# Performance work log

Hardware: AMD Instinct MI355X
Metric: run time of the kernel (lower is better)

Reference implementation:

```python
import jax, jax.numpy as jnp
import numpy as np
from jax import lax

NUM_HOP = 2      # opt.num_hop
POOL_HOP = 1     # Encoder(..., num_hop=1) in gnn_pools
K_POOL = 1024    # int(pooling_ratio * num_patches) = 0.5 * 2048
TH = 0.0         # opt.nonzero_th
T = 0.07         # NCE temperature
NEG_FILL = -10.0


def l2norm(x):
    # Normalize(power=2): x / (sum(x^2, dim=1, keepdim)^(1/2))
    return x / jnp.sqrt(jnp.sum(x * x, axis=1, keepdims=True))


def tagconv(A, h, W, b, k):
    # DGL TAGConv: concat_{i=0..k} (D^-1/2 A D^-1/2)^i h, then linear
    deg = jnp.sum(A, axis=1)
    dinv = lax.rsqrt(jnp.maximum(deg, 1e-12))
    An = A * dinv[:, None] * dinv[None, :]   # [N,N] normalized adjacency
    feats = [h]
    for _ in range(k):
        h = An @ h
        feats.append(h)
    return jnp.concatenate(feats, axis=1) @ W + b


def nce_pair(f_t, f_s):
    # calc_gnn NCE: positives = diag(f_t . f_s); negatives = full gram with diag masked to -10
    n = f_t.shape[0]
    eye = jnp.eye(n, dtype=bool)
    pos = jnp.sum(f_t * f_s, axis=1, keepdims=True)          # [N,1]
    neg_s = jnp.where(eye, NEG_FILL, f_t @ f_s.T)            # [N,N]
    neg_t = jnp.where(eye, NEG_FILL, f_s @ f_t.T)
    out_s = jnp.concatenate([pos, neg_s], axis=1) / T
    out_t = jnp.concatenate([pos, neg_t], axis=1) / T
    # CrossEntropy with label 0 == -log_softmax(out)[:, 0], mean over rows
    loss_s = -jnp.mean(jax.nn.log_softmax(out_s, axis=1)[:, 0])
    loss_t = -jnp.mean(jax.nn.log_softmax(out_t, axis=1)[:, 0])
    return loss_s + loss_t


def setup_inputs() -> dict:
    key = jax.random.key(0)
    ks = jax.random.split(key, 8)
    N, C, D = 2048, 512, 128
    g = 0.02  # init_gain ('normal' init)
    return {
        "fs": jax.random.normal(ks[0], (N, C), jnp.float32),
        "ft": jax.random.normal(ks[1], (N, C), jnp.float32),
        "W_embed": g * jax.random.normal(ks[2], (C, D), jnp.float32),
        "b_embed": jnp.zeros((D,), jnp.float32),
        "W_gnn": g * jax.random.normal(ks[3], ((NUM_HOP + 1) * D, D), jnp.float32),
        "b_gnn": jnp.zeros((D,), jnp.float32),
        "W_pool": g * jax.random.normal(ks[4], (D, 1), jnp.float32),
        "b_pool": jnp.zeros((1,), jnp.float32),
        "W_gnnp": g * jax.random.normal(ks[5], ((POOL_HOP + 1) * D, D), jnp.float32),
        "b_gnnp": jnp.zeros((D,), jnp.float32),
    }


def reference(fs, ft, W_embed, b_embed, W_gnn, b_gnn, W_pool, b_pool, W_gnnp, b_gnnp):
    # Embed: linear + l2 norm
    f_es = l2norm(fs @ W_embed + b_embed)   # student [N, nc]
    f_et = l2norm(ft @ W_embed + b_embed)   # teacher [N, nc]

    # nonzero_graph on detached teacher features; same adjacency reused for student
    ft_d = lax.stop_gradient(f_et)
    n = f_et.shape[0]
    eye = jnp.eye(n, dtype=bool)
    A = (ft_d @ ft_d.T > TH).astype(f_et.dtype)
    A = jnp.where(eye, 1.0, A)  # dgl.add_self_loop

    # TAGConv encoder + l2norm; teacher branch detached
    f_gt = lax.stop_gradient(l2norm(tagconv(A, f_et, W_gnn, b_gnn, NUM_HOP)))
    f_gs = l2norm(tagconv(A, f_es, W_gnn, b_gnn, NUM_HOP))
    loss_g = nce_pair(f_gt, f_gs)

    # Pool / top_k_graph
    scores = jax.nn.sigmoid((f_gt @ W_pool + b_pool)[:, 0])   # [N]
    vals, idx = lax.top_k(scores, K_POOL)
    new_ht = f_gt[idx] * vals[:, None]
    new_hs = f_gs[idx] * vals[:, None]
    un = (A > 0).astype(A.dtype)
    un2 = ((un @ un) > 0).astype(A.dtype)        # 2-hop boolean adjacency
    sub = un2[idx][:, idx]                       # [k,k]
    deg = jnp.sum(sub, axis=1)
    g_pool = sub / deg[None, :]                  # replicates torch broadcast in norm_g(g/degrees)

    # pooled-stage Encoder (TAGConv k=1) on the pooled graph structure (with self loops)
    k = K_POOL
    eye_k = jnp.eye(k, dtype=bool)
    Ap = (g_pool > 0).astype(A.dtype)
    Ap = jnp.where(eye_k, 1.0, Ap)
    f_pt = lax.stop_gradient(l2norm(tagconv(Ap, new_ht, W_gnnp, b_gnnp, POOL_HOP)))
    f_ps = l2norm(tagconv(Ap, new_hs, W_gnnp, b_gnnp, POOL_HOP))
    loss_pool = nce_pair(f_pt, f_ps)

    return loss_g + loss_pool
```

## Files before the change

kernel.cpp:

```cpp
#include <hip/hip_runtime.h>


#define TINV (1.0f / 0.07f)

using short8 = __attribute__((ext_vector_type(8))) short;
using f32x4  = __attribute__((ext_vector_type(4))) float;

__device__ __forceinline__ unsigned short f2bf(float f) {
    unsigned u = __float_as_uint(f);
    u += 0x7fff + ((u >> 16) & 1);
    return (unsigned short)(u >> 16);
}

template<bool BT>
__device__ __forceinline__ void mm_tile(const float* __restrict__ A, int lda,
                                        const float* __restrict__ B, int ldb,
                                        int i0, int j0, int k0, int k1,
                                        float (&acc)[4][4],
                                        float (&As)[16][68], float (&Bs)[16][68])
{
    const int tid = threadIdx.x;
    const int tx = tid & 15;
    const int ty = tid >> 4;
    const int lr = tid >> 2;
    const int lc = (tid & 3) * 4;
    for (int k = k0; k < k1; k += 16) {
        float4 av = *(const float4*)(A + (size_t)(i0 + lr) * lda + (k + lc));
        As[lc + 0][lr] = av.x; As[lc + 1][lr] = av.y;
        As[lc + 2][lr] = av.z; As[lc + 3][lr] = av.w;
        if (BT) {
            float4 bv = *(const float4*)(B + (size_t)(j0 + lr) * ldb + (k + lc));
            Bs[lc + 0][lr] = bv.x; Bs[lc + 1][lr] = bv.y;
            Bs[lc + 2][lr] = bv.z; Bs[lc + 3][lr] = bv.w;
        } else {
            const int n = tid & 63;
            const int kb = tid >> 6;
#pragma unroll
            for (int it = 0; it < 4; ++it)
                Bs[kb * 4 + it][n] = B[(size_t)(k + kb * 4 + it) * ldb + (j0 + n)];
        }
        __syncthreads();
#pragma unroll
        for (int kk = 0; kk < 16; ++kk) {
            float a[4], b[4];
#pragma unroll
            for (int u = 0; u < 4; ++u) a[u] = As[kk][ty * 4 + u];
#pragma unroll
            for (int v = 0; v < 4; ++v) b[v] = Bs[kk][tx * 4 + v];
#pragma unroll
            for (int u = 0; u < 4; ++u)
#pragma unroll
                for (int v = 0; v < 4; ++v)
                    acc[u][v] = fmaf(a[u], b[v], acc[u][v]);
// ... 70 lines not shown
    const int i0 = by * 64, j0 = bx * 64;
    float acc[4][4] = {};
    mm_tile<true>(f_e, 128, f_e, 128, i0, j0, 0, 128, acc, As, Bs);
    const int tid = threadIdx.x;
    const int tx = tid & 15, ty = tid >> 4;
    unsigned pb = 0;
#pragma unroll
    for (int u = 0; u < 4; ++u)
#pragma unroll
        for (int v = 0; v < 4; ++v) {
            bool pred = (acc[u][v] > 0.0f) || (i0 + ty * 4 + u == j0 + tx * 4 + v);
            pb |= (unsigned)pred << (u * 4 + v);
        }
#pragma unroll
    for (int u = 0; u < 4; ++u) nib[ty * 4 + u][tx] = (pb >> (4 * u)) & 15;
#pragma unroll
    for (int v = 0; v < 4; ++v) {
        unsigned nt = 0;
#pragma unroll
        for (int u = 0; u < 4; ++u) nt |= ((pb >> (u * 4 + v)) & 1u) << u;
        nibT[tx * 4 + v][ty] = nt;
    }
    __syncthreads();
    if (tid < 64) {
        unsigned long long c = 0;
#pragma unroll
        for (int t = 0; t < 16; ++t) c |= (unsigned long long)nib[tid][t] << (4 * t);
        chk[tid] = c;
        bits[(size_t)(i0 + tid) * 32 + (j0 >> 6)] = c;
        atomicAdd(&deg[i0 + tid], __popcll(c));
    } else if (tid < 128 && bx != by) {
        const int r = tid - 64;
        unsigned long long c = 0;
#pragma unroll
        for (int t = 0; t < 16; ++t) c |= (unsigned long long)nibT[r][t] << (4 * t);
        chkT[r] = c;
        bits[(size_t)(j0 + r) * 32 + (i0 >> 6)] = c;
        atomicAdd(&deg[j0 + r], __popcll(c));
    }
    __syncthreads();
#pragma unroll
    for (int it = 0; it < 16; ++it) {
        const int row = it * 4 + (tid >> 6);
        const int col = tid & 63;
        A01[(size_t)(i0 + row) * 2048 + j0 + col] =
            ((chk[row] >> col) & 1) ? (unsigned short)0x3F80 : (unsigned short)0;
        if (bx != by)
            A01[(size_t)(j0 + row) * 2048 + i0 + col] =
                ((chkT[row] >> col) & 1) ? (unsigned short)0x3F80 : (unsigned short)0;
    }
}

__launch_bounds__(256)
__global__ void mm_bf16(const unsigned short* __restrict__ A, int lda, size_t aZ,
                        const unsigned short* __restrict__ B, int ldb, size_t bZ,
                        float* __restrict__ C, int ldc, size_t cZ,
                        int Kc, int kZ)
{
    __shared__ unsigned short As[64][40];
    __shared__ unsigned short Bs[128][40];
    const int tid = threadIdx.x;
    const int bz = blockIdx.z;
    const int i0 = blockIdx.y * 64;
    const int j0 = blockIdx.x * 128;
    const int k0 = bz * kZ;
    const unsigned short* Ab = A + (size_t)bz * aZ;
    const unsigned short* Bb = B + (size_t)bz * bZ;
    float* Cb = C + (size_t)bz * cZ;
    const int w = tid >> 6;
    const int lane = tid & 63;
    const int m = lane & 15;
    const int q = lane >> 4;
    f32x4 acc[8];
#pragma unroll
    for (int t = 0; t < 8; ++t)
#pragma unroll
        for (int r = 0; r < 4; ++r) acc[t][r] = 0.0f;

    const int ar = tid >> 2;
    const int ac = (tid & 3) * 8;
    for (int ks = 0; ks < Kc; ks += 32) {
        const int k = k0 + ks;
        *(ulonglong2*)&As[ar][ac] =
            *(const ulonglong2*)(Ab + (size_t)(i0 + ar) * lda + k + ac);
        *(ulonglong2*)&Bs[ar][ac] =
            *(const ulonglong2*)(Bb + (size_t)(j0 + ar) * ldb + k + ac);
        *(ulonglong2*)&Bs[ar + 64][ac] =
            *(const ulonglong2*)(Bb + (size_t)(j0 + ar + 64) * ldb + k + ac);
        __syncthreads();
        short8 a = *(const short8*)&As[w * 16 + m][q * 8];
#pragma unroll
        for (int nt = 0; nt < 8; ++nt) {
            short8 b = *(const short8*)&Bs[nt * 16 + m][q * 8];
            acc[nt] = __builtin_amdgcn_mfma_f32_16x16x32_bf16(a, b, acc[nt], 0, 0, 0);
        }
        __syncthreads();
    }
#pragma unroll
    for (int nt = 0; nt < 8; ++nt) {
        const int col = j0 + nt * 16 + m;
#pragma unroll
        for (int r = 0; r < 4; ++r) {
            const int row = i0 + w * 16 + q * 4 + r;
            Cb[(size_t)row * ldc + col] = acc[nt][r];
        }
    }
}

__global__ void reduce_hop(const float* __restrict__ part, int nz, size_t zstr,
                           int M, const float* __restrict__ dinv,
                           unsigned short* __restrict__ hb,
                           unsigned short* __restrict__ xt)
{
    __shared__ float T[32][33];
    const int tid = threadIdx.x;
    const int iloc = tid >> 3, nq = (tid & 7) * 4;
    const int n = blockIdx.x * 32 + nq;
    const int i = blockIdx.y * 32 + iloc;
    float4 s = *(const float4*)(part + (size_t)i * 256 + n);
    for (int z = 1; z < nz; ++z) {
        float4 t = *(const float4*)(part + (size_t)z * zstr + (size_t)i * 256 + n);
        s.x += t.x; s.y += t.y; s.z += t.z; s.w += t.w;
    }
    const float d = dinv[i];
    unsigned short o[4] = { f2bf(s.x * d), f2bf(s.y * d), f2bf(s.z * d), f2bf(s.w * d) };
    const int hrow = (n >= 128 ? M : 0) + i;
    *(ulonglong1*)(hb + (size_t)hrow * 128 + (n & 127)) = *(ulonglong1*)o;
    if (xt) {
        const float d2 = d * d;
        T[nq + 0][iloc] = s.x * d2; T[nq + 1][iloc] = s.y * d2;
        T[nq + 2][iloc] = s.z * d2; T[nq + 3][iloc] = s.w * d2;
        __syncthreads();
        const int nloc = tid >> 3, ic = (tid & 7) * 4;
        unsigned short o2[4];
#pragma unroll
        for (int c = 0; c < 4; ++c) o2[c] = f2bf(T[nloc][ic + c]);
        *(ulonglong1*)(xt + (size_t)(blockIdx.x * 32 + nloc) * M + blockIdx.y * 32 + ic) =
            *(ulonglong1*)o2;
    }
}

__global__ void combine_norm(const float* __restrict__ part, int nz, size_t zstr,
                             const float* __restrict__ bias,
                             float* __restrict__ f32out,
                             unsigned short* __restrict__ bf16out,
                             const float* __restrict__ Wp, const float* __restrict__ bp,
                             float* __restrict__ scores)
{
    const int row = blockIdx.x;
    const int tid = threadIdx.x;
    float v = bias[tid];
    for (int z = 0; z < nz; ++z) v += part[(size_t)z * zstr + (size_t)row * 128 + tid];
    __shared__ float red[128];
    red[tid] = v * v;
    __syncthreads();
    for (int s = 64; s > 0; s >>= 1) {
        if (tid < s) red[tid] += red[tid + s];
        __syncthreads();
    }
    const float o = v * (1.0f / sqrtf(red[0]));
    if (f32out)  f32out[(size_t)row * 128 + tid] = o;
    if (bf16out) bf16out[(size_t)row * 128 + tid] = f2bf(o);
    if (scores && row < 2048) {
        __syncthreads();
        red[tid] = o * Wp[tid];
        __syncthreads();
        for (int s = 64; s > 0; s >>= 1) {
            if (tid < s) red[tid] += red[tid + s];
            __syncthreads();
        }
        if (tid == 0) scores[row] = 1.0f / (1.0f + expf(-(red[0] + bp[0])));
    }
}

__global__ void make_xt(const float* __restrict__ f_e, const int* __restrict__ deg,
                        unsigned short* __restrict__ xt, float* __restrict__ dinv)
{
    __shared__ float T[32][33];
    const int b = blockIdx.x;
    const int bx = b & 7, by = b >> 3;
    const int tid = threadIdx.x;
    const int iloc = tid >> 3, nq = (tid & 7) * 4;
    const int n0 = bx * 32;
    const int i = by * 32 + iloc;
    const int srow = (n0 >= 128 ? 2048 : 0) + i;
    float4 f = *(const float4*)(f_e + (size_t)srow * 128 + ((n0 + nq) & 127));
    const float d = 1.0f / sqrtf((float)deg[i]);
    if (bx == 0 && (tid & 7) == 0) dinv[i] = d;
    T[nq + 0][iloc] = f.x * d; T[nq + 1][iloc] = f.y * d;
    T[nq + 2][iloc] = f.z * d; T[nq + 3][iloc] = f.w * d;
    __syncthreads();
    const int nloc = tid >> 3, ic = (tid & 7) * 4;
    unsigned short o[4];
#pragma unroll
    for (int c = 0; c < 4; ++c) o[c] = f2bf(T[nloc][ic + c]);
    *(ulonglong1*)(xt + (size_t)(n0 + nloc) * 2048 + by * 32 + ic) = *(ulonglong1*)o;
}

__launch_bounds__(256)
__global__ void k_nce_topk(const unsigned short* __restrict__ A,
                           const unsigned short* __restrict__ B,
                           float* __restrict__ rowsum, float* __restrict__ colsum,
                           float* __restrict__ pos, int gramBlocks, int bw,
                           const float* __restrict__ scores,
                           float* __restrict__ vals, int* __restrict__ idx)
{
    __shared__ unsigned short As[64][40];
    __shared__ unsigned short Bs[128][40];
    __shared__ float colbuf[4][128];
    __shared__ unsigned sv[2048];
    __shared__ int hist[256];
    __shared__ int shp, shr, sh_base, sh_out, wsum[5];
    const int tid = threadIdx.x;
    const int b = blockIdx.x;
    if (b < gramBlocks) {
        const int bx = b % bw, by = b / bw;
        const int i0 = by * 64;
        const int j0 = bx * 128;
        const int w = tid >> 6;
        const int lane = tid & 63;
        const int m = lane & 15;
        const int q = lane >> 4;
        f32x4 acc[8];
#pragma unroll
        for (int t = 0; t < 8; ++t)
#pragma unroll
            for (int r = 0; r < 4; ++r) acc[t][r] = 0.0f;
        const int ar = tid >> 2;
        const int ac = (tid & 3) * 8;
        for (int k = 0; k < 128; k += 32) {
            *(ulonglong2*)&As[ar][ac] =
                *(const ulonglong2*)(A + (size_t)(i0 + ar) * 128 + k + ac);
            *(ulonglong2*)&Bs[ar][ac] =
                *(const ulonglong2*)(B + (size_t)(j0 + ar) * 128 + k + ac);
            *(ulonglong2*)&Bs[ar + 64][ac] =
                *(const ulonglong2*)(B + (size_t)(j0 + ar + 64) * 128 + k + ac);
            __syncthreads();
            short8 a = *(const short8*)&As[w * 16 + m][q * 8];
#pragma unroll
            for (int nt = 0; nt < 8; ++nt) {
                short8 bb = *(const short8*)&Bs[nt * 16 + m][q * 8];
                acc[nt] = __builtin_amdgcn_mfma_f32_16x16x32_bf16(a, bb, acc[nt], 0, 0, 0);
            }
            __syncthreads();
        }
        float rpart[4] = {0.0f, 0.0f, 0.0f, 0.0f};
        float cpart[8];
#pragma unroll
        for (int nt = 0; nt < 8; ++nt) {
            const int col = j0 + nt * 16 + m;
            float cs = 0.0f;
#pragma unroll
            for (int r = 0; r < 4; ++r) {
                const int row = i0 + w * 16 + q * 4 + r;
                float g = acc[nt][r];
                float e = __expf(g * TINV);
                if (row == col) { pos[row] = g; e = 0.0f; }
                rpart[r] += e;
                cs += e;
            }
            cpart[nt] = cs;
        }
#pragma unroll
        for (int r = 0; r < 4; ++r) {
            float v = rpart[r];
            v += __shfl_xor(v, 1); v += __shfl_xor(v, 2);
            v += __shfl_xor(v, 4); v += __shfl_xor(v, 8);
            if (m == 0) atomicAdd(&rowsum[i0 + w * 16 + q * 4 + r], v);
        }
#pragma unroll
        for (int nt = 0; nt < 8; ++nt) {
            float v = cpart[nt];
            v += __shfl_xor(v, 16); v += __shfl_xor(v, 32);
            if (q == 0) colbuf[w][nt * 16 + m] = v;
        }
        __syncthreads();
        if (tid < 128) {
            float v = colbuf[0][tid] + colbuf[1][tid] + colbuf[2][tid] + colbuf[3][tid];
            atomicAdd(&colsum[j0 + tid], v);
        }
    } else {
        for (int e = tid; e < 2048; e += 256) sv[e] = __float_as_uint(scores[e]);
        if (tid == 0) { shp = 0; shr = 1024; sh_base = 0; sh_out = 0; }
        __syncthreads();
        for (int byte = 3; byte >= 0; --byte) {
            hist[tid] = 0;
            __syncthreads();
            const unsigned pref = (unsigned)shp;
            const unsigned pmask = (byte == 3) ? 0u : (0xFFFFFFFFu << ((byte + 1) * 8));
            for (int e = tid; e < 2048; e += 256) {
                unsigned u = sv[e];
                if ((u & pmask) == (pref & pmask))
                    atomicAdd(&hist[(u >> (byte * 8)) & 255], 1);
            }
            __syncthreads();
            if (tid == 0) {
                int rem = shr, bs = 255;
                for (; bs > 0; --bs) {
                    if (hist[bs] >= rem) break;
                    rem -= hist[bs];
                }
                shp = (int)(pref | ((unsigned)bs << (byte * 8)));
                shr = rem;
            }
            __syncthreads();
        }
        const unsigned t = (unsigned)shp;
        const int remain = shr;
        const int lane = tid & 63, wave = tid >> 6;
        for (int pass = 0; pass < 8; ++pass) {
            const int e = pass * 256 + tid;
            const unsigned u = sv[e];
            const bool eq = (u == t);
            unsigned long long mk = __ballot(eq);
            int wpre = __popcll(mk & ((1ull << lane) - 1ull));
            if (lane == 0) wsum[wave] = __popcll(mk);
            __syncthreads();
            if (tid == 0) {
                int a = sh_base;
                for (int ww = 0; ww < 4; ++ww) { int c = wsum[ww]; wsum[ww] = a; a += c; }
                sh_base = a;
            }
            __syncthreads();
            const int rank = eq ? (wsum[wave] + wpre) : 0x7fffffff;
            if ((u > t) || (eq && rank < remain)) {
                int slot = atomicAdd(&sh_out, 1);
                idx[slot] = e;
                vals[slot] = __uint_as_float(u);
            }
            __syncthreads();
        }
    }
}

__global__ void k_final_ap(const float* __restrict__ rs, const float* __restrict__ cs,
                           const float* __restrict__ pos, float* __restrict__ out,
                           const unsigned long long* __restrict__ bits,
                           const int* __restrict__ idx,
                           unsigned short* __restrict__ Ap, int* __restrict__ degp)
{
    __shared__ unsigned long long pb[16][33];
    __shared__ unsigned long long qb[16][33];
    __shared__ float red[256];
    const int b = blockIdx.x;
    const int tid = threadIdx.x;
    if (b < 4096) {
        const int tp = (b >> 6) * 16;
        const int tq = (b & 63) * 16;
        for (int t = tid; t < 512; t += 256) {
            int r = t >> 5, w = t & 31;
            pb[r][w] = bits[(size_t)idx[tp + r] * 32 + w];
            qb[r][w] = bits[(size_t)idx[tq + r] * 32 + w];
        }
        __syncthreads();
        const int pi = tid >> 4, qi = tid & 15;
        unsigned long long acc = 0;
#pragma unroll
        for (int w = 0; w < 32; ++w) acc |= (pb[pi][w] & qb[qi][w]);
        Ap[(size_t)(tp + pi) * 1024 + tq + qi] =
            acc ? (unsigned short)0x3F80 : (unsigned short)0;
        int v = acc ? 1 : 0;
        v += __shfl_xor(v, 1); v += __shfl_xor(v, 2);
        v += __shfl_xor(v, 4); v += __shfl_xor(v, 8);
        if (qi == 0) atomicAdd(&degp[tp + pi], v);
    } else {
        const int i = (b - 4096) * 256 + tid;
        float p = pos[i] * TINV;
        float ep = __expf(p);
        float t = (logf(rs[i] + ep) - p) + (logf(cs[i] + ep) - p);
        red[tid] = t;
        __syncthreads();
        for (int s = 128; s > 0; s >>= 1) {
            if (tid < s) red[tid] += red[tid + s];
            __syncthreads();
        }
        if (tid == 0) atomicAdd(out, red[0] * (1.0f / 2048.0f));
    }
}

__global__ void nce_final(const float* __restrict__ rs, const float* __restrict__ cs,
                          const float* __restrict__ pos, float invN,
                          float* __restrict__ out)
{
    const int i = blockIdx.x * 256 + threadIdx.x;
    float p = pos[i] * TINV;
    float ep = __expf(p);
    float t = (logf(rs[i] + ep) - p) + (logf(cs[i] + ep) - p);
    __shared__ float red[256];
    red[threadIdx.x] = t;
    __syncthreads();
    for (int s = 128; s > 0; s >>= 1) {
        if (threadIdx.x < s) red[threadIdx.x] += red[threadIdx.x + s];
        __syncthreads();
    }
    if (threadIdx.x == 0) atomicAdd(out, red[0] * invN);
}

__global__ void gather_xt(const float* __restrict__ f_g, const int* __restrict__ idx,
                          const float* __restrict__ vals, const int* __restrict__ degp,
                          unsigned short* __restrict__ new_hb,
                          unsigned short* __restrict__ xtp, float* __restrict__ dinvp)
{
    __shared__ float T[32][33];
    const int b = blockIdx.x;
    const int bx = b & 7, by = b >> 3;
    const int tid = threadIdx.x;
    const int ploc = tid >> 3, nq = (tid & 7) * 4;
    const int n0 = bx * 32;
    const int p = by * 32 + ploc;
    const int s = idx[p];
    const float v = vals[p];
    const float dp = 1.0f / sqrtf((float)degp[p]);
    if (bx == 0 && (tid & 7) == 0) dinvp[p] = dp;
    const int srow = (n0 >= 128 ? 2048 : 0) + s;
    float4 f = *(const float4*)(f_g + (size_t)srow * 128 + ((n0 + nq) & 127));
    f.x *= v; f.y *= v; f.z *= v; f.w *= v;
    unsigned short o[4] = { f2bf(f.x), f2bf(f.y), f2bf(f.z), f2bf(f.w) };
    const int hrow = (n0 >= 128 ? 1024 : 0) + p;
    *(ulonglong1*)(new_hb + (size_t)hrow * 128 + ((n0 + nq) & 127)) = *(ulonglong1*)o;
    T[nq + 0][ploc] = f.x * dp; T[nq + 1][ploc] = f.y * dp;
    T[nq + 2][ploc] = f.z * dp; T[nq + 3][ploc] = f.w * dp;
    __syncthreads();
    const int nloc = tid >> 3, pc = (tid & 7) * 4;
    unsigned short o2[4];
#pragma unroll
    for (int c = 0; c < 4; ++c) o2[c] = f2bf(T[nloc][pc + c]);
    *(ulonglong1*)(xtp + (size_t)(n0 + nloc) * 1024 + by * 32 + pc) = *(ulonglong1*)o2;
}

extern "C" void kernel_launch(void* const* d_in, const int* in_sizes, int n_in,
                              void* d_out, int out_size, void* d_ws, size_t ws_size,
                              hipStream_t stream)
{
    (void)in_sizes; (void)n_in; (void)out_size; (void)ws_size;
    const float* fs      = (const float*)d_in[0];
    const float* ft      = (const float*)d_in[1];
    const float* W_embed = (const float*)d_in[2];
    const float* b_embed = (const float*)d_in[3];
    const float* W_gnn   = (const float*)d_in[4];
    const float* b_gnn   = (const float*)d_in[5];
    const float* W_pool  = (const float*)d_in[6];
    const float* b_pool  = (const float*)d_in[7];
    const float* W_gnnp  = (const float*)d_in[8];
    const float* b_gnnp  = (const float*)d_in[9];
    float* out = (float*)d_out;

    float* ws = (float*)d_ws;
    size_t o = 0;
    auto alloc = [&](size_t n) { float* p = ws + o; o += (n + 3) & ~3ull; return p; };
    float* bigB   = alloc(2048ull * 2048);
    float* f_e    = alloc(4096 * 128);
    float* f_g    = alloc(4096 * 128);
    unsigned short* A01  = (unsigned short*)alloc(2048ull * 2048 / 2);
    unsigned short* febT = (unsigned short*)alloc(3ull * 4096 * 128 / 2);
    unsigned short* Xt1  = (unsigned short*)alloc(256ull * 2048 / 2);
    unsigned short* Xt2  = (unsigned short*)alloc(256ull * 2048 / 2);
    unsigned short* f_gb = (unsigned short*)alloc(4096ull * 128 / 2);
    unsigned short* Wtall= (unsigned short*)alloc(5ull * 16384 / 2);
    unsigned short* Ap01 = (unsigned short*)alloc(1024ull * 1024 / 2);
    unsigned short* nhb  = (unsigned short*)alloc(2ull * 2048 * 128 / 2);
    unsigned short* Xtp  = (unsigned short*)alloc(256ull * 1024 / 2);
    unsigned short* f_pb = (unsigned short*)alloc(2048ull * 128 / 2);
    float* dinv   = alloc(2048);
    float* scores = alloc(2048);
    float* vals   = alloc(1024);
    int*   idxb   = (int*)alloc(1024);
    float* dinvp  = alloc(1024);
    unsigned long long* bits = (unsigned long long*)alloc(2048 * 32 * 2);
    float* nceb = alloc(9216);
    int*   deg  = (int*)alloc(2048);
    int*   degp = (int*)alloc(1024);
    const int kZeroCount = 9216 + 2048 + 1024;

    const size_t FSTR = 4096ull * 128;
    const size_t PSTR = 1024ull * 256;
    unsigned short* feb = febT;
    unsigned short* h1b = febT + FSTR;
    unsigned short* h2b = febT + 2 * FSTR;
    unsigned short* tmpb = nhb + 2048ull * 128;
    unsigned short* Wt  = Wtall;
    unsigned short* WtP = Wtall + 3ull * 16384;
    float* rs  = nceb;
    float* csu = nceb + 2048;
    float* pos = nceb + 4096;
    float* rsp  = nceb + 6144;
    float* csp  = nceb + 7168;
    float* posp = nceb + 8192;

    k_setup_embed<<<601, 256, 0, stream>>>(fs, ft, W_embed, bigB, FSTR,
                                           (int*)nceb, kZeroCount, out, W_gnn, W_gnnp, Wtall);
    combine_norm<<<4096, 128, 0, stream>>>(bigB, 4, FSTR, b_embed, f_e, feb,
                                           nullptr, nullptr, nullptr);
    k_gram_fused<<<528, 256, 0, stream>>>(f_e, A01, bits, deg);
    make_xt<<<512, 256, 0, stream>>>(f_e, deg, Xt1, dinv);
    mm_bf16<<<dim3(2, 32, 8), 256, 0, stream>>>(A01, 2048, 0, Xt1, 2048, 0,
                                                bigB, 256, FSTR, 256, 256);
    reduce_hop<<<dim3(8, 64), 256, 0, stream>>>(bigB, 8, FSTR, 2048, dinv, h1b, Xt2);
    mm_bf16<<<dim3(2, 32, 8), 256, 0, stream>>>(A01, 2048, 0, Xt2, 2048, 0,
                                                bigB, 256, FSTR, 256, 256);
    reduce_hop<<<dim3(8, 64), 256, 0, stream>>>(bigB, 8, FSTR, 2048, dinv, h2b, nullptr);
    mm_bf16<<<dim3(1, 64, 3), 256, 0, stream>>>(feb, 128, FSTR, Wt, 128, 16384,
                                                bigB, 128, FSTR, 128, 0);
    combine_norm<<<4096, 128, 0, stream>>>(bigB, 3, FSTR, b_gnn, f_g, f_gb,
                                           W_pool, b_pool, scores);
    k_nce_topk<<<513, 256, 0, stream>>>(f_gb, f_gb + 2048 * 128, rs, csu, pos,
                                        512, 16, scores, vals, idxb);
    k_final_ap<<<4104, 256, 0, stream>>>(rs, csu, pos, out, bits, idxb, Ap01, degp);
    gather_xt<<<256, 256, 0, stream>>>(f_g, idxb, vals, degp, nhb, Xtp, dinvp);
    mm_bf16<<<dim3(2, 16, 8), 256, 0, stream>>>(Ap01, 1024, 0, Xtp, 1024, 0,
                                                bigB, 256, PSTR, 128, 128);
    reduce_hop<<<dim3(8, 32), 256, 0, stream>>>(bigB, 8, PSTR, 1024, dinvp, tmpb, nullptr);
    mm_bf16<<<dim3(1, 32, 2), 256, 0, stream>>>(nhb, 128, 2048ull * 128, WtP, 128, 16384,
                                                bigB, 128, PSTR, 128, 0);
    combine_norm<<<2048, 128, 0, stream>>>(bigB, 2, PSTR, b_gnnp, nullptr, f_pb,
                                           nullptr, nullptr, nullptr);
    k_nce_topk<<<128, 256, 0, stream>>>(f_pb, f_pb + 1024 * 128, rsp, csp, posp,
                                        128, 8, nullptr, nullptr, nullptr);
    nce_final<<<4, 256, 0, stream>>>(rsp, csp, posp, 1.0f / 1024.0f, out);
}
```

Baseline: 227.3 us.

## Fuse pooled-stage kernels into one cooperative persistent kernel with grid syncs

Replaces the seven small kernels of the pooled stage (gather, adjacency matmul, hop reduction, weight matmul, normalize, NCE gram, final reduction) with one cooperative kernel of 256 blocks that separates the phases with grid.sync(). The aim is to remove per-kernel launch gaps and tail latency on stages that are each tiny. In exchange the phases run on a fixed 256-block grid with some blocks idle, grid-wide barriers add their own cost, and the launch requires cooperative co-residency. The NCE gram tile code is also moved into a shared device function.

```diff
diff --git a/kernel.cpp b/kernel.cpp
--- a/kernel.cpp
+++ b/kernel.cpp
@@ -1,4 +1,7 @@
 #include <hip/hip_runtime.h>
+#include <hip/hip_cooperative_groups.h>
+
+namespace cg = cooperative_groups;
 
 
 #define TINV (1.0f / 0.07f)
@@ -320,11 +323,86 @@
     *(ulonglong1*)(xt + (size_t)(n0 + nloc) * 2048 + by * 32 + ic) = *(ulonglong1*)o;
 }
 
+__device__ __forceinline__ void nce_gram_tile(const unsigned short* __restrict__ A,
+                                              const unsigned short* __restrict__ B,
+                                              int i0, int j0,
+                                              float* __restrict__ rowsum,
+                                              float* __restrict__ colsum,
+                                              float* __restrict__ pos,
+                                              unsigned short (&As)[64][40],
+                                              unsigned short (&Bs)[128][40],
+                                              float (&colbuf)[4][128])
+{
+    const int tid = threadIdx.x;
+    const int w = tid >> 6;
+    const int lane = tid & 63;
+    const int m = lane & 15;
+    const int q = lane >> 4;
+    f32x4 acc[8];
+#pragma unroll
+    for (int t = 0; t < 8; ++t)
+#pragma unroll
+        for (int r = 0; r < 4; ++r) acc[t][r] = 0.0f;
+    const int ar = tid >> 2;
+    const int ac = (tid & 3) * 8;
+    for (int k = 0; k < 128; k += 32) {
+        *(ulonglong2*)&As[ar][ac] =
+            *(const ulonglong2*)(A + (size_t)(i0 + ar) * 128 + k + ac);
+        *(ulonglong2*)&Bs[ar][ac] =
+            *(const ulonglong2*)(B + (size_t)(j0 + ar) * 128 + k + ac);
+        *(ulonglong2*)&Bs[ar + 64][ac] =
+            *(const ulonglong2*)(B + (size_t)(j0 + ar + 64) * 128 + k + ac);
+        __syncthreads();
+        short8 a = *(const short8*)&As[w * 16 + m][q * 8];
+#pragma unroll
+        for (int nt = 0; nt < 8; ++nt) {
+            short8 bb = *(const short8*)&Bs[nt * 16 + m][q * 8];
+            acc[nt] = __builtin_amdgcn_mfma_f32_16x16x32_bf16(a, bb, acc[nt], 0, 0, 0);
+        }
+        __syncthreads();
+    }
+    float rpart[4] = {0.0f, 0.0f, 0.0f, 0.0f};
+    float cpart[8];
+#pragma unroll
+    for (int nt = 0; nt < 8; ++nt) {
+        const int col = j0 + nt * 16 + m;
+        float cs = 0.0f;
+#pragma unroll
+        for (int r = 0; r < 4; ++r) {
+            const int row = i0 + w * 16 + q * 4 + r;
+            float g = acc[nt][r];
+            float e = __expf(g * TINV);
+            if (row == col) { pos[row] = g; e = 0.0f; }
+            rpart[r] += e;
+            cs += e;
+        }
+        cpart[nt] = cs;
+    }
+#pragma unroll
+    for (int r = 0; r < 4; ++r) {
+        float v = rpart[r];
+        v += __shfl_xor(v, 1); v += __shfl_xor(v, 2);
+        v += __shfl_xor(v, 4); v += __shfl_xor(v, 8);
+        if (m == 0) atomicAdd(&rowsum[i0 + w * 16 + q * 4 + r], v);
+    }
+#pragma unroll
+    for (int nt = 0; nt < 8; ++nt) {
+        float v = cpart[nt];
+        v += __shfl_xor(v, 16); v += __shfl_xor(v, 32);
+        if (q == 0) colbuf[w][nt * 16 + m] = v;
+    }
+    __syncthreads();
+    if (tid < 128) {
+        float v = colbuf[0][tid] + colbuf[1][tid] + colbuf[2][tid] + colbuf[3][tid];
+        atomicAdd(&colsum[j0 + tid], v);
+    }
+}
+
 __launch_bounds__(256)
 __global__ void k_nce_topk(const unsigned short* __restrict__ A,
                            const unsigned short* __restrict__ B,
                            float* __restrict__ rowsum, float* __restrict__ colsum,
-                           float* __restrict__ pos, int gramBlocks, int bw,
+                           float* __restrict__ pos,
                            const float* __restrict__ scores,
                            float* __restrict__ vals, int* __restrict__ idx)
 {
@@ -336,72 +414,9 @@
     __shared__ int shp, shr, sh_base, sh_out, wsum[5];
     const int tid = threadIdx.x;
     const int b = blockIdx.x;
-    if (b < gramBlocks) {
-        const int bx = b % bw, by = b / bw;
-        const int i0 = by * 64;
-        const int j0 = bx * 128;
-        const int w = tid >> 6;
-        const int lane = tid & 63;
-        const int m = lane & 15;
-        const int q = lane >> 4;
-        f32x4 acc[8];
-#pragma unroll
-        for (int t = 0; t < 8; ++t)
-#pragma unroll
-            for (int r = 0; r < 4; ++r) acc[t][r] = 0.0f;
-        const int ar = tid >> 2;
-        const int ac = (tid & 3) * 8;
-        for (int k = 0; k < 128; k += 32) {
-            *(ulonglong2*)&As[ar][ac] =
-                *(const ulonglong2*)(A + (size_t)(i0 + ar) * 128 + k + ac);
-            *(ulonglong2*)&Bs[ar][ac] =
-                *(const ulonglong2*)(B + (size_t)(j0 + ar) * 128 + k + ac);
-            *(ulonglong2*)&Bs[ar + 64][ac] =
-                *(const ulonglong2*)(B + (size_t)(j0 + ar + 64) * 128 + k + ac);
-            __syncthreads();
-            short8 a = *(const short8*)&As[w * 16 + m][q * 8];
-#pragma unroll
-            for (int nt = 0; nt < 8; ++nt) {
-                short8 bb = *(const short8*)&Bs[nt * 16 + m][q * 8];
-                acc[nt] = __builtin_amdgcn_mfma_f32_16x16x32_bf16(a, bb, acc[nt], 0, 0, 0);
-            }
-            __syncthreads();
-        }
-        float rpart[4] = {0.0f, 0.0f, 0.0f, 0.0f};
-        float cpart[8];
-#pragma unroll
-        for (int nt = 0; nt < 8; ++nt) {
-            const int col = j0 + nt * 16 + m;
-            float cs = 0.0f;
-#pragma unroll
-            for (int r = 0; r < 4; ++r) {
-                const int row = i0 + w * 16 + q * 4 + r;
-                float g = acc[nt][r];
-                float e = __expf(g * TINV);
-                if (row == col) { pos[row] = g; e = 0.0f; }
-                rpart[r] += e;
-                cs += e;
-            }
-            cpart[nt] = cs;
-        }
-#pragma unroll
-        for (int r = 0; r < 4; ++r) {
-            float v = rpart[r];
-            v += __shfl_xor(v, 1); v += __shfl_xor(v, 2);
-            v += __shfl_xor(v, 4); v += __shfl_xor(v, 8);
-            if (m == 0) atomicAdd(&rowsum[i0 + w * 16 + q * 4 + r], v);
-        }
-#pragma unroll
-        for (int nt = 0; nt < 8; ++nt) {
-            float v = cpart[nt];
-            v += __shfl_xor(v, 16); v += __shfl_xor(v, 32);
-            if (q == 0) colbuf[w][nt * 16 + m] = v;
-        }
-        __syncthreads();
-        if (tid < 128) {
-            float v = colbuf[0][tid] + colbuf[1][tid] + colbuf[2][tid] + colbuf[3][tid];
-            atomicAdd(&colsum[j0 + tid], v);
-        }
+    if (b < 512) {
+        nce_gram_tile(A, B, (b / 16) * 64, (b % 16) * 128, rowsum, colsum, pos,
+                      As, Bs, colbuf);
     } else {
         for (int e = tid; e < 2048; e += 256) sv[e] = __float_as_uint(scores[e]);
         if (tid == 0) { shp = 0; shr = 1024; sh_base = 0; sh_out = 0; }
@@ -501,54 +516,188 @@
     }
 }
 
-__global__ void nce_final(const float* __restrict__ rs, const float* __restrict__ cs,
-                          const float* __restrict__ pos, float invN,
-                          float* __restrict__ out)
-{
-    const int i = blockIdx.x * 256 + threadIdx.x;
-    float p = pos[i] * TINV;
-    float ep = __expf(p);
-    float t = (logf(rs[i] + ep) - p) + (logf(cs[i] + ep) - p);
+__launch_bounds__(256)
+__global__ void k_pooled(const float* __restrict__ f_g, const int* __restrict__ idx,
+                         const float* __restrict__ vals, const int* __restrict__ degp,
+                         unsigned short* __restrict__ new_hb,
+                         unsigned short* __restrict__ xtp,
+                         float* __restrict__ dinvp,
+                         const unsigned short* __restrict__ Ap,
+                         float* __restrict__ partb,
+                         unsigned short* __restrict__ tmpb,
+                         const unsigned short* __restrict__ WtP,
+                         const float* __restrict__ bgp,
+                         unsigned short* __restrict__ f_pb,
+                         float* __restrict__ rsp, float* __restrict__ csp,
+                         float* __restrict__ posp, float* __restrict__ out)
+{
+    cg::grid_group grid = cg::this_grid();
+    __shared__ unsigned short As[64][40];
+    __shared__ unsigned short Bs[128][40];
+    __shared__ float colbuf[4][128];
+    __shared__ float T[32][33];
     __shared__ float red[256];
-    red[threadIdx.x] = t;
-    __syncthreads();
-    for (int s = 128; s > 0; s >>= 1) {
-        if (threadIdx.x < s) red[threadIdx.x] += red[threadIdx.x + s];
-        __syncthreads();
-    }
-    if (threadIdx.x == 0) atomicAdd(out, red[0] * invN);
-}
-
-__global__ void gather_xt(const float* __restrict__ f_g, const int* __restrict__ idx,
-                          const float* __restrict__ vals, const int* __restrict__ degp,
-                          unsigned short* __restrict__ new_hb,
-                          unsigned short* __restrict__ xtp, float* __restrict__ dinvp)
-{
-    __shared__ float T[32][33];
     const int b = blockIdx.x;
-    const int bx = b & 7, by = b >> 3;
-    const int tid = threadIdx.x;
-    const int ploc = tid >> 3, nq = (tid & 7) * 4;
-    const int n0 = bx * 32;
-    const int p = by * 32 + ploc;
-    const int s = idx[p];
-    const float v = vals[p];
-    const float dp = 1.0f / sqrtf((float)degp[p]);
-    if (bx == 0 && (tid & 7) == 0) dinvp[p] = dp;
-    const int srow = (n0 >= 128 ? 2048 : 0) + s;
-    float4 f = *(const float4*)(f_g + (size_t)srow * 128 + ((n0 + nq) & 127));
-    f.x *= v; f.y *= v; f.z *= v; f.w *= v;
-    unsigned short o[4] = { f2bf(f.x), f2bf(f.y), f2bf(f.z), f2bf(f.w) };
-    const int hrow = (n0 >= 128 ? 1024 : 0) + p;
-    *(ulonglong1*)(new_hb + (size_t)hrow * 128 + ((n0 + nq) & 127)) = *(ulonglong1*)o;
-    T[nq + 0][ploc] = f.x * dp; T[nq + 1][ploc] = f.y * dp;
-    T[nq + 2][ploc] = f.z * dp; T[nq + 3][ploc] = f.w * dp;
-    __syncthreads();
-    const int nloc = tid >> 3, pc = (tid & 7) * 4;
-    unsigned short o2[4];
-#pragma unroll
-    for (int c = 0; c < 4; ++c) o2[c] = f2bf(T[nloc][pc + c]);
-    *(ulonglong1*)(xtp + (size_t)(n0 + nloc) * 1024 + by * 32 + pc) = *(ulonglong1*)o2;
+    const int tid = threadIdx.x;
+    const size_t PSTR = 1024ull * 256;
+
+    {
+        const int bx = b & 7, by = b >> 3;
+        const int ploc = tid >> 3, nq = (tid & 7) * 4;
+        const int n0 = bx * 32;
+        const int p = by * 32 + ploc;
+        const int s = idx[p];
+        const float v = vals[p];
+        const float dp = 1.0f / sqrtf((float)degp[p]);
+        if (bx == 0 && (tid & 7) == 0) dinvp[p] = dp;
+        const int srow = (n0 >= 128 ? 2048 : 0) + s;
+        float4 f = *(const float4*)(f_g + (size_t)srow * 128 + ((n0 + nq) & 127));
+        f.x *= v; f.y *= v; f.z *= v; f.w *= v;
+        unsigned short o[4] = { f2bf(f.x), f2bf(f.y), f2bf(f.z), f2bf(f.w) };
+        const int hrow = (n0 >= 128 ? 1024 : 0) + p;
+        *(ulonglong1*)(new_hb + (size_t)hrow * 128 + ((n0 + nq) & 127)) = *(ulonglong1*)o;
+        T[nq + 0][ploc] = f.x * dp; T[nq + 1][ploc] = f.y * dp;
+        T[nq + 2][ploc] = f.z * dp; T[nq + 3][ploc] = f.w * dp;
+        __syncthreads();
+        const int nloc = tid >> 3, pc = (tid & 7) * 4;
+        unsigned short o2[4];
+#pragma unroll
+        for (int c = 0; c < 4; ++c) o2[c] = f2bf(T[nloc][pc + c]);
+        *(ulonglong1*)(xtp + (size_t)(n0 + nloc) * 1024 + by * 32 + pc) = *(ulonglong1*)o2;
+    }
+    grid.sync();
+
+    {
+        const int bx = b & 1, by = (b >> 1) & 15, bz = b >> 5;
+        const int i0 = by * 64, j0 = bx * 128, k0 = bz * 128;
+        float* Cb = partb + (size_t)bz * PSTR;
+        const int w = tid >> 6, lane = tid & 63, m = lane & 15, q = lane >> 4;
+        f32x4 acc[8];
+#pragma unroll
+        for (int t = 0; t < 8; ++t)
+#pragma unroll
+            for (int r = 0; r < 4; ++r) acc[t][r] = 0.0f;
+        const int ar = tid >> 2, ac = (tid & 3) * 8;
+        for (int ks = 0; ks < 128; ks += 32) {
+            const int k = k0 + ks;
+            *(ulonglong2*)&As[ar][ac] =
+                *(const ulonglong2*)(Ap + (size_t)(i0 + ar) * 1024 + k + ac);
+            *(ulonglong2*)&Bs[ar][ac] =
+                *(const ulonglong2*)(xtp + (size_t)(j0 + ar) * 1024 + k + ac);
+            *(ulonglong2*)&Bs[ar + 64][ac] =
+                *(const ulonglong2*)(xtp + (size_t)(j0 + ar + 64) * 1024 + k + ac);
+            __syncthreads();
+            short8 a = *(const short8*)&As[w * 16 + m][q * 8];
+#pragma unroll
+            for (int nt = 0; nt < 8; ++nt) {
+                short8 bb = *(const short8*)&Bs[nt * 16 + m][q * 8];
+                acc[nt] = __builtin_amdgcn_mfma_f32_16x16x32_bf16(a, bb, acc[nt], 0, 0, 0);
+            }
+            __syncthreads();
+        }
+#pragma unroll
+        for (int nt = 0; nt < 8; ++nt) {
+            const int col = j0 + nt * 16 + m;
+#pragma unroll
+            for (int r = 0; r < 4; ++r)
+                Cb[(size_t)(i0 + w * 16 + q * 4 + r) * 256 + col] = acc[nt][r];
+        }
+    }
+    grid.sync();
+
+    {
+        const int bx = b & 7, by = b >> 3;
+        const int iloc = tid >> 3, nq = (tid & 7) * 4;
+        const int n = bx * 32 + nq;
+        const int i = by * 32 + iloc;
+        float4 s = *(const float4*)(partb + (size_t)i * 256 + n);
+        for (int z = 1; z < 8; ++z) {
+            float4 t = *(const float4*)(partb + (size_t)z * PSTR + (size_t)i * 256 + n);
+            s.x += t.x; s.y += t.y; s.z += t.z; s.w += t.w;
+        }
+        const float d = dinvp[i];
+        unsigned short o[4] = { f2bf(s.x * d), f2bf(s.y * d), f2bf(s.z * d), f2bf(s.w * d) };
+        const int hrow = (n >= 128 ? 1024 : 0) + i;
+        *(ulonglong1*)(tmpb + (size_t)hrow * 128 + (n & 127)) = *(ulonglong1*)o;
+    }
+    grid.sync();
+
+    if (b < 64) {
+        const int bz = b >> 5, by = b & 31;
+        const int i0 = by * 64, j0 = 0;
+        const unsigned short* Abase = (bz == 0) ? new_hb : tmpb;
+        const unsigned short* Wb = WtP + (size_t)bz * 16384;
+        float* Cb = partb + (size_t)bz * PSTR;
+        const int w = tid >> 6, lane = tid & 63, m = lane & 15, q = lane >> 4;
+        f32x4 acc[8];
+#pragma unroll
+        for (int t = 0; t < 8; ++t)
+#pragma unroll
+            for (int r = 0; r < 4; ++r) acc[t][r] = 0.0f;
+        const int ar = tid >> 2, ac = (tid & 3) * 8;
+        for (int ks = 0; ks < 128; ks += 32) {
+            *(ulonglong2*)&As[ar][ac] =
+                *(const ulonglong2*)(Abase + (size_t)(i0 + ar) * 128 + ks + ac);
+            *(ulonglong2*)&Bs[ar][ac] =
+                *(const ulonglong2*)(Wb + (size_t)(j0 + ar) * 128 + ks + ac);
+            *(ulonglong2*)&Bs[ar + 64][ac] =
+                *(const ulonglong2*)(Wb + (size_t)(j0 + ar + 64) * 128 + ks + ac);
+            __syncthreads();
+            short8 a = *(const short8*)&As[w * 16 + m][q * 8];
+#pragma unroll
+            for (int nt = 0; nt < 8; ++nt) {
+                short8 bb = *(const short8*)&Bs[nt * 16 + m][q * 8];
+                acc[nt] = __builtin_amdgcn_mfma_f32_16x16x32_bf16(a, bb, acc[nt], 0, 0, 0);
+            }
+            __syncthreads();
+        }
+#pragma unroll
+        for (int nt = 0; nt < 8; ++nt) {
+            const int col = j0 + nt * 16 + m;
+#pragma unroll
+            for (int r = 0; r < 4; ++r)
+                Cb[(size_t)(i0 + w * 16 + q * 4 + r) * 128 + col] = acc[nt][r];
+        }
+    }
+    grid.sync();
+
+    {
+        const int sub = tid >> 7, l = tid & 127;
+        for (int it = 0; it < 4; ++it) {
+            const int row = b * 8 + it * 2 + sub;
+            float v = bgp[l] + partb[(size_t)row * 128 + l]
+                            + partb[PSTR + (size_t)row * 128 + l];
+            red[tid] = v * v;
+            __syncthreads();
+            for (int s = 64; s > 0; s >>= 1) {
+                if (l < s) red[sub * 128 + l] += red[sub * 128 + l + s];
+                __syncthreads();
+            }
+            f_pb[(size_t)row * 128 + l] = f2bf(v * (1.0f / sqrtf(red[sub * 128])));
+            __syncthreads();
+        }
+    }
+    grid.sync();
+
+    if (b < 128) {
+        nce_gram_tile(f_pb, f_pb + 1024 * 128, (b >> 3) * 64, (b & 7) * 128,
+                      rsp, csp, posp, As, Bs, colbuf);
+    }
+    grid.sync();
+
+    if (b < 4) {
+        const int i = b * 256 + tid;
+        float p = posp[i] * TINV;
+        float ep = __expf(p);
+        float t = (logf(rsp[i] + ep) - p) + (logf(csp[i] + ep) - p);
+        red[tid] = t;
+        __syncthreads();
+        for (int s = 128; s > 0; s >>= 1) {
+            if (tid < s) red[tid] += red[tid + s];
+            __syncthreads();
+        }
+        if (tid == 0) atomicAdd(out, red[0] * (1.0f / 1024.0f));
+    }
 }
 
 extern "C" void kernel_launch(void* const* d_in, const int* in_sizes, int n_in,
@@ -596,7 +745,6 @@
     const int kZeroCount = 9216 + 2048 + 1024;
 
     const size_t FSTR = 4096ull * 128;
-    const size_t PSTR = 1024ull * 256;
     unsigned short* feb = febT;
     unsigned short* h1b = febT + FSTR;
     unsigned short* h2b = febT + 2 * FSTR;
@@ -627,17 +775,15 @@
     combine_norm<<<4096, 128, 0, stream>>>(bigB, 3, FSTR, b_gnn, f_g, f_gb,
                                            W_pool, b_pool, scores);
     k_nce_topk<<<513, 256, 0, stream>>>(f_gb, f_gb + 2048 * 128, rs, csu, pos,
-                                        512, 16, scores, vals, idxb);
+                                        scores, vals, idxb);
     k_final_ap<<<4104, 256, 0, stream>>>(rs, csu, pos, out, bits, idxb, Ap01, degp);
-    gather_xt<<<256, 256, 0, stream>>>(f_g, idxb, vals, degp, nhb, Xtp, dinvp);
-    mm_bf16<<<dim3(2, 16, 8), 256, 0, stream>>>(Ap01, 1024, 0, Xtp, 1024, 0,
-                                                bigB, 256, PSTR, 128, 128);
-    reduce_hop<<<dim3(8, 32), 256, 0, stream>>>(bigB, 8, PSTR, 1024, dinvp, tmpb, nullptr);
-    mm_bf16<<<dim3(1, 32, 2), 256, 0, stream>>>(nhb, 128, 2048ull * 128, WtP, 128, 16384,
-                                                bigB, 128, PSTR, 128, 0);
-    combine_norm<<<2048, 128, 0, stream>>>(bigB, 2, PSTR, b_gnnp, nullptr, f_pb,
-                                           nullptr, nullptr, nullptr);
-    k_nce_topk<<<128, 256, 0, stream>>>(f_pb, f_pb + 1024 * 128, rsp, csp, posp,
-                                        128, 8, nullptr, nullptr, nullptr);
-    nce_final<<<4, 256, 0, stream>>>(rsp, csp, posp, 1.0f / 1024.0f, out);
-}
+    {
+        void* args[] = { (void*)&f_g, (void*)&idxb, (void*)&vals, (void*)&degp,
+                         (void*)&nhb, (void*)&Xtp, (void*)&dinvp, (void*)&Ap01,
+                         (void*)&bigB, (void*)&tmpb, (void*)&WtP, (void*)&b_gnnp,
+                         (void*)&f_pb, (void*)&rsp, (void*)&csp, (void*)&posp,
+                         (void*)&out };
+        hipLaunchCooperativeKernel((void*)k_pooled, dim3(256), dim3(256),
+                                   args, 0, stream);
+    }
+}
```

Measured after the change: 415.3 us. 82.7% more time.

## Fuse TAGConv linear projection with bias, L2 norm and pool scoring

Applied to the files above, without the earlier changes.

Replaces the split-K bf16 GEMM plus combine_norm pair for both TAGConv output projections with one MFMA kernel. It accumulates all hop sources against the weight slices in registers, then applies bias, row L2 normalisation and the sigmoid pool score in the epilogue. This removes the fp32 partial-sum round trip through global memory and one kernel launch per stage. In exchange, only 64 or 32 workgroups run, which may underfill the GPU, and the output stores are strided scalar writes.

```diff
diff --git a/kernel.cpp b/kernel.cpp
--- a/kernel.cpp
+++ b/kernel.cpp
@@ -266,9 +266,7 @@
 __global__ void combine_norm(const float* __restrict__ part, int nz, size_t zstr,
                              const float* __restrict__ bias,
                              float* __restrict__ f32out,
-                             unsigned short* __restrict__ bf16out,
-                             const float* __restrict__ Wp, const float* __restrict__ bp,
-                             float* __restrict__ scores)
+                             unsigned short* __restrict__ bf16out)
 {
     const int row = blockIdx.x;
     const int tid = threadIdx.x;
@@ -284,15 +282,103 @@
     const float o = v * (1.0f / sqrtf(red[0]));
     if (f32out)  f32out[(size_t)row * 128 + tid] = o;
     if (bf16out) bf16out[(size_t)row * 128 + tid] = f2bf(o);
-    if (scores && row < 2048) {
-        __syncthreads();
-        red[tid] = o * Wp[tid];
-        __syncthreads();
-        for (int s = 64; s > 0; s >>= 1) {
-            if (tid < s) red[tid] += red[tid + s];
-            __syncthreads();
-        }
-        if (tid == 0) scores[row] = 1.0f / (1.0f + expf(-(red[0] + bp[0])));
+}
+
+__launch_bounds__(256)
+__global__ void k_tag_fused(const unsigned short* __restrict__ A0,
+                            const unsigned short* __restrict__ A1,
+                            const unsigned short* __restrict__ A2,
+                            const unsigned short* __restrict__ Wt,
+                            const float* __restrict__ bias, int nsrc,
+                            float* __restrict__ f32out,
+                            unsigned short* __restrict__ bf16out,
+                            const float* __restrict__ Wp,
+                            const float* __restrict__ bp,
+                            float* __restrict__ scores)
+{
+    __shared__ unsigned short As[64][40];
+    __shared__ unsigned short Bs[128][40];
+    const int tid = threadIdx.x;
+    const int i0 = blockIdx.x * 64;
+    const int w = tid >> 6;
+    const int lane = tid & 63;
+    const int m = lane & 15;
+    const int q = lane >> 4;
+    f32x4 acc[8];
+#pragma unroll
+    for (int t = 0; t < 8; ++t)
+#pragma unroll
+        for (int r = 0; r < 4; ++r) acc[t][r] = 0.0f;
+
+    const int ar = tid >> 2;
+    const int ac = (tid & 3) * 8;
+    for (int s = 0; s < nsrc; ++s) {
+        const unsigned short* A = (s == 0) ? A0 : (s == 1) ? A1 : A2;
+        const unsigned short* W = Wt + (size_t)s * 16384;
+        for (int ks = 0; ks < 128; ks += 32) {
+            *(ulonglong2*)&As[ar][ac] =
+                *(const ulonglong2*)(A + (size_t)(i0 + ar) * 128 + ks + ac);
+            *(ulonglong2*)&Bs[ar][ac] =
+                *(const ulonglong2*)(W + (size_t)ar * 128 + ks + ac);
+            *(ulonglong2*)&Bs[ar + 64][ac] =
+                *(const ulonglong2*)(W + (size_t)(ar + 64) * 128 + ks + ac);
+            __syncthreads();
+            short8 a = *(const short8*)&As[w * 16 + m][q * 8];
+#pragma unroll
+            for (int nt = 0; nt < 8; ++nt) {
+                short8 b = *(const short8*)&Bs[nt * 16 + m][q * 8];
+                acc[nt] = __builtin_amdgcn_mfma_f32_16x16x32_bf16(a, b, acc[nt], 0, 0, 0);
+            }
+            __syncthreads();
+        }
+    }
+    float ov[8][4];
+    float sq[4] = {0.0f, 0.0f, 0.0f, 0.0f};
+#pragma unroll
+    for (int nt = 0; nt < 8; ++nt) {
+        const float bcol = bias[nt * 16 + m];
+#pragma unroll
+        for (int r = 0; r < 4; ++r) {
+            float v = acc[nt][r] + bcol;
+            ov[nt][r] = v;
+            sq[r] += v * v;
+        }
+    }
+    float rn[4];
+#pragma unroll
+    for (int r = 0; r < 4; ++r) {
+        float v = sq[r];
+        v += __shfl_xor(v, 1); v += __shfl_xor(v, 2);
+        v += __shfl_xor(v, 4); v += __shfl_xor(v, 8);
+        rn[r] = 1.0f / sqrtf(v);
+    }
+#pragma unroll
+    for (int nt = 0; nt < 8; ++nt) {
+        const int col = nt * 16 + m;
+#pragma unroll
+        for (int r = 0; r < 4; ++r) {
+            const int row = i0 + w * 16 + q * 4 + r;
+            const float val = ov[nt][r] * rn[r];
+            if (f32out)  f32out[(size_t)row * 128 + col] = val;
+            bf16out[(size_t)row * 128 + col] = f2bf(val);
+        }
+    }
+    if (scores && i0 < 2048) {
+        float sc[4] = {0.0f, 0.0f, 0.0f, 0.0f};
+#pragma unroll
+        for (int nt = 0; nt < 8; ++nt) {
+            const float wcol = Wp[nt * 16 + m];
+#pragma unroll
+            for (int r = 0; r < 4; ++r) sc[r] += ov[nt][r] * rn[r] * wcol;
+        }
+#pragma unroll
+        for (int r = 0; r < 4; ++r) {
+            float v = sc[r];
+            v += __shfl_xor(v, 1); v += __shfl_xor(v, 2);
+            v += __shfl_xor(v, 4); v += __shfl_xor(v, 8);
+            if (m == 0)
+                scores[i0 + w * 16 + q * 4 + r] = 1.0f / (1.0f + expf(-(v + bp[0])));
+        }
     }
 }
 
@@ -612,8 +698,7 @@
 
     k_setup_embed<<<601, 256, 0, stream>>>(fs, ft, W_embed, bigB, FSTR,
                                            (int*)nceb, kZeroCount, out, W_gnn, W_gnnp, Wtall);
-    combine_norm<<<4096, 128, 0, stream>>>(bigB, 4, FSTR, b_embed, f_e, feb,
-                                           nullptr, nullptr, nullptr);
+    combine_norm<<<4096, 128, 0, stream>>>(bigB, 4, FSTR, b_embed, f_e, feb);
     k_gram_fused<<<528, 256, 0, stream>>>(f_e, A01, bits, deg);
     make_xt<<<512, 256, 0, stream>>>(f_e, deg, Xt1, dinv);
     mm_bf16<<<dim3(2, 32, 8), 256, 0, stream>>>(A01, 2048, 0, Xt1, 2048, 0,
@@ -622,10 +707,8 @@
     mm_bf16<<<dim3(2, 32, 8), 256, 0, stream>>>(A01, 2048, 0, Xt2, 2048, 0,
                                                 bigB, 256, FSTR, 256, 256);
     reduce_hop<<<dim3(8, 64), 256, 0, stream>>>(bigB, 8, FSTR, 2048, dinv, h2b, nullptr);
-    mm_bf16<<<dim3(1, 64, 3), 256, 0, stream>>>(feb, 128, FSTR, Wt, 128, 16384,
-                                                bigB, 128, FSTR, 128, 0);
-    combine_norm<<<4096, 128, 0, stream>>>(bigB, 3, FSTR, b_gnn, f_g, f_gb,
-                                           W_pool, b_pool, scores);
+    k_tag_fused<<<64, 256, 0, stream>>>(feb, h1b, h2b, Wt, b_gnn, 3,
+                                        f_g, f_gb, W_pool, b_pool, scores);
     k_nce_topk<<<513, 256, 0, stream>>>(f_gb, f_gb + 2048 * 128, rs, csu, pos,
                                         512, 16, scores, vals, idxb);
     k_final_ap<<<4104, 256, 0, stream>>>(rs, csu, pos, out, bits, idxb, Ap01, degp);
@@ -633,10 +716,8 @@
     mm_bf16<<<dim3(2, 16, 8), 256, 0, stream>>>(Ap01, 1024, 0, Xtp, 1024, 0,
                                                 bigB, 256, PSTR, 128, 128);
     reduce_hop<<<dim3(8, 32), 256, 0, stream>>>(bigB, 8, PSTR, 1024, dinvp, tmpb, nullptr);
-    mm_bf16<<<dim3(1, 32, 2), 256, 0, stream>>>(nhb, 128, 2048ull * 128, WtP, 128, 16384,
-                                                bigB, 128, PSTR, 128, 0);
-    combine_norm<<<2048, 128, 0, stream>>>(bigB, 2, PSTR, b_gnnp, nullptr, f_pb,
-                                           nullptr, nullptr, nullptr);
+    k_tag_fused<<<32, 256, 0, stream>>>(nhb, tmpb, nullptr, WtP, b_gnnp, 2,
+                                        nullptr, f_pb, nullptr, nullptr, nullptr);
     k_nce_topk<<<128, 256, 0, stream>>>(f_pb, f_pb + 1024 * 128, rsp, csp, posp,
                                         128, 8, nullptr, nullptr, nullptr);
     nce_final<<<4, 256, 0, stream>>>(rsp, csp, posp, 1.0f / 1024.0f, out);
```

Result: no change. 231.5 us (+1.9%).

## Fuse split-K hop matmul and reduction into single full-K kernel

Applied to the files above, without the earlier changes.

Replaces the split-K mm_bf16 plus reduce_hop pair for each adjacency propagation hop with a single k_hop kernel. Each block computes a 64x32 output tile over the full K dimension, then applies the dinv scaling, bf16 conversion and transposed Xt write from shared memory in its epilogue. This removes the fp32 partial-sum round trip through global memory and one launch per hop. In exchange each block runs a long serial K loop with only two MFMA tiles per wave and no software pipelining, and there are fewer blocks (256 or 128).

```diff
diff --git a/kernel.cpp b/kernel.cpp
--- a/kernel.cpp
+++ b/kernel.cpp
@@ -175,6 +175,79 @@
 }
 
 __launch_bounds__(256)
+__global__ void k_hop(const unsigned short* __restrict__ A, int lda,
+                      const unsigned short* __restrict__ B, int ldb,
+                      int M, int K, const float* __restrict__ dinv,
+                      unsigned short* __restrict__ hb,
+                      unsigned short* __restrict__ xt)
+{
+    __shared__ unsigned short As[64][40];
+    __shared__ unsigned short Bs[32][40];
+    __shared__ float T[64][33];
+    const int tid = threadIdx.x;
+    const int i0 = blockIdx.y * 64;
+    const int j0 = blockIdx.x * 32;
+    const int w = tid >> 6;
+    const int lane = tid & 63;
+    const int m = lane & 15;
+    const int q = lane >> 4;
+    f32x4 acc[2];
+#pragma unroll
+    for (int t = 0; t < 2; ++t)
+#pragma unroll
+        for (int r = 0; r < 4; ++r) acc[t][r] = 0.0f;
+
+    const int ar = tid >> 2;
+    const int ac = (tid & 3) * 8;
+    for (int k = 0; k < K; k += 32) {
+        *(ulonglong2*)&As[ar][ac] =
+            *(const ulonglong2*)(A + (size_t)(i0 + ar) * lda + k + ac);
+        if (tid < 128) {
+            const int br = tid >> 2;
+            const int bc = (tid & 3) * 8;
+            *(ulonglong2*)&Bs[br][bc] =
+                *(const ulonglong2*)(B + (size_t)(j0 + br) * ldb + k + bc);
+        }
+        __syncthreads();
+        short8 a = *(const short8*)&As[w * 16 + m][q * 8];
+#pragma unroll
+        for (int nt = 0; nt < 2; ++nt) {
+            short8 b = *(const short8*)&Bs[nt * 16 + m][q * 8];
+            acc[nt] = __builtin_amdgcn_mfma_f32_16x16x32_bf16(a, b, acc[nt], 0, 0, 0);
+        }
+        __syncthreads();
+    }
+#pragma unroll
+    for (int nt = 0; nt < 2; ++nt)
+#pragma unroll
+        for (int r = 0; r < 4; ++r)
+            T[w * 16 + q * 4 + r][nt * 16 + m] = acc[nt][r];
+    __syncthreads();
+    {
+        const int r = tid >> 2;
+        const int c0 = (tid & 3) * 8;
+        const float d = dinv[i0 + r];
+        unsigned short o[8];
+#pragma unroll
+        for (int c = 0; c < 8; ++c) o[c] = f2bf(T[r][c0 + c] * d);
+        const int branch = (j0 >= 128) ? M : 0;
+        *(ulonglong2*)&hb[(size_t)(branch + i0 + r) * 128 + (j0 & 127) + c0] =
+            *(ulonglong2*)o;
+    }
+    if (xt) {
+        const int c = tid >> 3;
+        const int r0 = (tid & 7) * 8;
+        unsigned short o[8];
+#pragma unroll
+        for (int rr = 0; rr < 8; ++rr) {
+            const float d = dinv[i0 + r0 + rr];
+            o[rr] = f2bf(T[r0 + rr][c] * d * d);
+        }
+        *(ulonglong2*)&xt[(size_t)(j0 + c) * M + i0 + r0] = *(ulonglong2*)o;
+    }
+}
+
+__launch_bounds__(256)
 __global__ void mm_bf16(const unsigned short* __restrict__ A, int lda, size_t aZ,
                         const unsigned short* __restrict__ B, int ldb, size_t bZ,
                         float* __restrict__ C, int ldc, size_t cZ,
@@ -227,39 +300,6 @@
             const int row = i0 + w * 16 + q * 4 + r;
             Cb[(size_t)row * ldc + col] = acc[nt][r];
         }
-    }
-}
-
-__global__ void reduce_hop(const float* __restrict__ part, int nz, size_t zstr,
-                           int M, const float* __restrict__ dinv,
-                           unsigned short* __restrict__ hb,
-                           unsigned short* __restrict__ xt)
-{
-    __shared__ float T[32][33];
-    const int tid = threadIdx.x;
-    const int iloc = tid >> 3, nq = (tid & 7) * 4;
-    const int n = blockIdx.x * 32 + nq;
-    const int i = blockIdx.y * 32 + iloc;
-    float4 s = *(const float4*)(part + (size_t)i * 256 + n);
-    for (int z = 1; z < nz; ++z) {
-        float4 t = *(const float4*)(part + (size_t)z * zstr + (size_t)i * 256 + n);
-        s.x += t.x; s.y += t.y; s.z += t.z; s.w += t.w;
-    }
-    const float d = dinv[i];
-    unsigned short o[4] = { f2bf(s.x * d), f2bf(s.y * d), f2bf(s.z * d), f2bf(s.w * d) };
-    const int hrow = (n >= 128 ? M : 0) + i;
-    *(ulonglong1*)(hb + (size_t)hrow * 128 + (n & 127)) = *(ulonglong1*)o;
-    if (xt) {
-        const float d2 = d * d;
-        T[nq + 0][iloc] = s.x * d2; T[nq + 1][iloc] = s.y * d2;
-        T[nq + 2][iloc] = s.z * d2; T[nq + 3][iloc] = s.w * d2;
-        __syncthreads();
-        const int nloc = tid >> 3, ic = (tid & 7) * 4;
-        unsigned short o2[4];
-#pragma unroll
-        for (int c = 0; c < 4; ++c) o2[c] = f2bf(T[nloc][ic + c]);
-        *(ulonglong1*)(xt + (size_t)(blockIdx.x * 32 + nloc) * M + blockIdx.y * 32 + ic) =
-            *(ulonglong1*)o2;
     }
 }
 
@@ -616,12 +656,10 @@
                                            nullptr, nullptr, nullptr);
     k_gram_fused<<<528, 256, 0, stream>>>(f_e, A01, bits, deg);
     make_xt<<<512, 256, 0, stream>>>(f_e, deg, Xt1, dinv);
-    mm_bf16<<<dim3(2, 32, 8), 256, 0, stream>>>(A01, 2048, 0, Xt1, 2048, 0,
-                                                bigB, 256, FSTR, 256, 256);
-    reduce_hop<<<dim3(8, 64), 256, 0, stream>>>(bigB, 8, FSTR, 2048, dinv, h1b, Xt2);
-    mm_bf16<<<dim3(2, 32, 8), 256, 0, stream>>>(A01, 2048, 0, Xt2, 2048, 0,
-                                                bigB, 256, FSTR, 256, 256);
-    reduce_hop<<<dim3(8, 64), 256, 0, stream>>>(bigB, 8, FSTR, 2048, dinv, h2b, nullptr);
+    k_hop<<<dim3(8, 32), 256, 0, stream>>>(A01, 2048, Xt1, 2048, 2048, 2048,
+                                           dinv, h1b, Xt2);
+    k_hop<<<dim3(8, 32), 256, 0, stream>>>(A01, 2048, Xt2, 2048, 2048, 2048,
+                                           dinv, h2b, nullptr);
     mm_bf16<<<dim3(1, 64, 3), 256, 0, stream>>>(feb, 128, FSTR, Wt, 128, 16384,
                                                 bigB, 128, FSTR, 128, 0);
     combine_norm<<<4096, 128, 0, stream>>>(bigB, 3, FSTR, b_gnn, f_g, f_gb,
@@ -630,9 +668,8 @@
                                         512, 16, scores, vals, idxb);
     k_final_ap<<<4104, 256, 0, stream>>>(rs, csu, pos, out, bits, idxb, Ap01, degp);
     gather_xt<<<256, 256, 0, stream>>>(f_g, idxb, vals, degp, nhb, Xtp, dinvp);
-    mm_bf16<<<dim3(2, 16, 8), 256, 0, stream>>>(Ap01, 1024, 0, Xtp, 1024, 0,
-                                                bigB, 256, PSTR, 128, 128);
-    reduce_hop<<<dim3(8, 32), 256, 0, stream>>>(bigB, 8, PSTR, 1024, dinvp, tmpb, nullptr);
+    k_hop<<<dim3(8, 16), 256, 0, stream>>>(Ap01, 1024, Xtp, 1024, 1024, 1024,
+                                           dinvp, tmpb, nullptr);
     mm_bf16<<<dim3(1, 32, 2), 256, 0, stream>>>(nhb, 128, 2048ull * 128, WtP, 128, 16384,
                                                 bigB, 128, PSTR, 128, 0);
     combine_norm<<<2048, 128, 0, stream>>>(bigB, 2, PSTR, b_gnnp, nullptr, f_pb,
```

Measured after the change: 263.6 us. 16.0% more time.
